# Performance work log

Measured on AMD Instinct MI355X. Metric: run time of the kernel, lower is better.

Reference implementation:

```python
import jax, jax.numpy as jnp
import numpy as np

B, T, D, H, L = 64, 512, 1024, 1024, 4


def setup_inputs() -> dict:
    key = jax.random.key(0)
    ks = jax.random.split(key, 7)
    s = 1.0 / np.sqrt(H)
    x = jax.random.normal(ks[0], (B, T, D), dtype=jnp.float32)
    dt = jax.random.uniform(ks[1], (B, T), dtype=jnp.float32)  # positive time deltas
    W_ih = jax.random.uniform(ks[2], (L, 3 * H, D), minval=-s, maxval=s, dtype=jnp.float32)
    W_hh = jax.random.uniform(ks[3], (L, 3 * H, H), minval=-s, maxval=s, dtype=jnp.float32)
    b_ih = jax.random.uniform(ks[4], (L, 3 * H), minval=-s, maxval=s, dtype=jnp.float32)
    b_hh = jax.random.uniform(ks[5], (L, 3 * H), minval=-s, maxval=s, dtype=jnp.float32)
    tau = jax.random.uniform(ks[6], (L, H), minval=0.5, maxval=2.0, dtype=jnp.float32)
    return {"x": x, "dt": dt, "W_ih": W_ih, "W_hh": W_hh, "b_ih": b_ih, "b_hh": b_hh, "tau": tau}


def reference(x, dt, W_ih, W_hh, b_ih, b_hh, tau):
    # x: [B,T,D], dt: [B,T]; stacked per-layer params: W_ih [L,3H,D], W_hh [L,3H,H],
    # b_ih/b_hh [L,3H], tau [L,H] (learned time constants, 'exp' scaling).
    n_layers = W_hh.shape[0]
    hid = W_hh.shape[2]
    inv_tau = 1.0 / jax.nn.softplus(tau)  # [L,H]

    def step(h, xt):
        # h: [B,L,H]; x_t: [B,D]; dt_t: [B]
        x_t, dt_t = xt
        inp = x_t
        new_h = []
        for i in range(n_layers):  # fixed small layer count
            decay = jnp.exp(-dt_t[:, None] * inv_tau[i])        # [B,H] exp time scaling
            hd = h[:, i] * decay
            gx = inp @ W_ih[i].T + b_ih[i]                       # [B,3H]
            gh = hd @ W_hh[i].T + b_hh[i]                        # [B,3H]
            xr, xz, xn = jnp.split(gx, 3, axis=-1)
            hr, hz, hn = jnp.split(gh, 3, axis=-1)
            r = jax.nn.sigmoid(xr + hr)
            z = jax.nn.sigmoid(xz + hz)
            n = jnp.tanh(xn + r * hn)
            h_i = (1.0 - z) * n + z * hd                         # torch GRU convention
            new_h.append(h_i)
            inp = h_i
        return jnp.stack(new_h, axis=1), new_h[-1]

    h0 = jnp.zeros((x.shape[0], n_layers, hid), dtype=x.dtype)
    xs = (jnp.swapaxes(x, 0, 1), jnp.swapaxes(dt, 0, 1))  # time-major for scan
    _, seq = jax.lax.scan(step, h0, xs)                    # seq: [T,B,H]
    return jnp.swapaxes(seq, 0, 1)                         # [B,T,H]
```

## Files before the change

kernel.cpp:

```cpp
#include <hip/hip_runtime.h>

typedef _Float16 f16;
typedef _Float16 half8 __attribute__((ext_vector_type(8)));
typedef float f32x4 __attribute__((ext_vector_type(4)));
typedef float f32x2 __attribute__((ext_vector_type(2)));

#define TT 512
#define HID 1024

#define GLOAD_LDS16(gp, lp) \
  __builtin_amdgcn_global_load_lds((const __attribute__((address_space(1))) void*)(gp), \
                                   (__attribute__((address_space(3))) void*)(lp), 16, 0, 0)

__device__ __forceinline__ half8 cvt8(f32x4 lo, f32x4 hi) {
  half8 r;
  r[0]=(f16)lo[0]; r[1]=(f16)lo[1]; r[2]=(f16)lo[2]; r[3]=(f16)lo[3];
  r[4]=(f16)hi[0]; r[5]=(f16)hi[1]; r[6]=(f16)hi[2]; r[7]=(f16)hi[3];
  return r;
}
__device__ __forceinline__ void st_sc_u32(unsigned* p, unsigned v) {
  asm volatile("global_store_dword %0, %1, off sc0 sc1" :: "v"(p), "v"(v) : "memory");
}
__device__ __forceinline__ unsigned ld_sc_u32(const unsigned* p) {
  unsigned v;
  asm volatile("global_load_dword %0, %1, off sc0 sc1\n\ts_waitcnt vmcnt(0)"
               : "=v"(v) : "v"(p) : "memory");
  return v;
}
__device__ __forceinline__ void spinFlag(const unsigned* p) {
  int gd = 0;
  while (ld_sc_u32(p) == 0u) { __builtin_amdgcn_s_sleep(1); if (++gd > (1<<20)) break; }
}
__device__ __forceinline__ float sigm(float x)  { return 1.f/(1.f + __expf(-x)); }
__device__ __forceinline__ float ftanh(float x) { return 1.f - 2.f/(1.f + __expf(2.f*x)); }

__global__ void init_misc(const float* __restrict__ x, f16* __restrict__ xh) {
  size_t i = ((size_t)blockIdx.x*256 + threadIdx.x)*8;
  f32x4 a = *(const f32x4*)(x+i);
  f32x4 b = *(const f32x4*)(x+i+4);
  *(half8*)(xh+i) = cvt8(a,b);
}

__global__ __launch_bounds__(512, 2) void tsgru_k(
    const float* __restrict__ dtp, const float* __restrict__ Wih,
    const float* __restrict__ Whh, const float* __restrict__ bih,
    const float* __restrict__ bhh, const float* __restrict__ tau,
    const f16* __restrict__ xh, f16* __restrict__ H, f16* __restrict__ HD,
    unsigned* __restrict__ flags, float* __restrict__ out) {
  extern __shared__ char lds[];
  float* PART = (float*)lds;

  const int tid = threadIdx.x, lane = tid & 63, wv = tid >> 6;
  const int g = wv >> 2, kq = wv & 3;
  const int wg = blockIdx.x, layer = wg >> 6, wgl = wg & 63, col0 = wgl*16;
  const int l5 = lane >> 5, su = lane & 31;

  const float* Wsrc = (g ? Whh : Wih) + (size_t)layer*3072*HID;
  const int wrow = col0 + (lane & 15);
  const int kfr = kq*32 + ((lane>>4)&3)*8;
  half8 bW[3][8];
  #pragma unroll
  for (int q=0;q<3;q++)
    #pragma unroll
    for (int kc=0;kc<8;kc++) {
      const float* p = Wsrc + (size_t)(q*HID + wrow)*HID + kc*128 + kfr;
      bW[q][kc] = cvt8(*(const f32x4*)p, *(const f32x4*)(p+4));
    }

  const int gb = tid >> 3, gc2 = (tid & 7)*2;
  float biR[2],biZ[2],biN[2],bhR[2],bhZ[2],bhN[2],ni[2];
  #pragma unroll
  for (int e=0;e<2;e++) {
    const int c = col0 + gc2 + e;
    biR[e]=bih[layer*3072+c]; biZ[e]=bih[layer*3072+1024+c]; biN[e]=bih[layer*3072+2048+c];
    bhR[e]=bhh[layer*3072+c]; bhZ[e]=bhh[layer*3072+1024+c]; bhN[e]=bhh[layer*3072+2048+c];
    ni[e] = -1.0f / log1pf(expf(tau[layer*HID + c]));
  }

  const f16* agB; size_t agRS;
  if (layer == 0) { agB = xh; agRS = (size_t)TT*HID; }
  else            { agB = H + (size_t)(layer-1)*TT*65536; agRS = (size_t)HID; }
  f16* HDl = HD + (size_t)layer*2*65536;
  unsigned* flagOwn = flags + (size_t)layer*TT*64;
  const unsigned* flagUp = flags + (size_t)(layer>0 ? layer-1 : 0)*TT*64;

  float hdv0 = 0.f, hdv1 = 0.f;

  for (int t = 0; t < TT; ++t) {
    const float dtg1 = (t < TT-1) ? dtp[gb*TT + t + 1] : 0.f;

    if (t > 0 && lane != wgl) spinFlag(flagOwn + (size_t)(t-1)*64 + lane);
    if (layer > 0)            spinFlag(flagUp  + (size_t)t*64 + lane);

    const f16* agT = (layer==0) ? agB + (size_t)t*HID : agB + (size_t)t*65536;
    const f16* ahT = HDl + (size_t)(t & 1)*65536;

    auto issueQ = [&](int q, int par) {
      const int qo = q*256;
      #pragma unroll
      for (int i=0;i<4;i++) {
        const int b  = wv*8 + 2*i + l5;
        const int sw = (su ^ (2*i + l5)) * 8;
        char* ld0 = lds + par*32768 + (wv*8 + 2*i)*512;
        GLOAD_LDS16(agT + (size_t)b*agRS + qo + sw, ld0);
        GLOAD_LDS16(ahT + (size_t)b*HID  + qo + sw, ld0 + 65536);
      }
    };

    issueQ(0,0); issueQ(1,1);
    asm volatile("s_waitcnt vmcnt(8)" ::: "memory");
    __builtin_amdgcn_s_barrier();

    f32x4 acc[4][3];
    #pragma unroll
    for (int m=0;m<4;m++) { acc[m][0]=(f32x4){0.f,0.f,0.f,0.f}; acc[m][1]=acc[m][0]; acc[m][2]=acc[m][0]; }

    const char* AbB = lds + (g ? 65536 : 0);
    #pragma unroll
    for (int q=0;q<4;q++) {
      const char* Ab = AbB + (q&1)*32768;
      #pragma unroll
      for (int kcq=0;kcq<2;kcq++) {
        const int ub = kcq*16 + kq*4 + ((lane>>4)&3);
        const int kc = q*2 + kcq;
        #pragma unroll
        for (int m=0;m<4;m++) {
          const int row = m*16 + (lane&15);
          const half8 aF = *(const half8*)(Ab + row*512 + ((ub ^ (row&7))*16));
          acc[m][0] = __builtin_amdgcn_mfma_f32_16x16x32_f16(aF, bW[0][kc], acc[m][0],0,0,0);
          acc[m][1] = __builtin_amdgcn_mfma_f32_16x16x32_f16(aF, bW[1][kc], acc[m][1],0,0,0);
          acc[m][2] = __builtin_amdgcn_mfma_f32_16x16x32_f16(aF, bW[2][kc], acc[m][2],0,0,0);
        }
      }
      if (q < 2) {
        __builtin_amdgcn_s_barrier();
        issueQ(q+2, q&1);
        asm volatile("s_waitcnt vmcnt(8)" ::: "memory");
        __builtin_amdgcn_s_barrier();
      } else if (q == 2) {
        asm volatile("s_waitcnt vmcnt(0)" ::: "memory");
        __builtin_amdgcn_s_barrier();
      }
    }
    __builtin_amdgcn_s_barrier();

    {
      float* Pb = PART + (size_t)((g*4+kq)*3)*1088 + (lane&15)*68 + ((lane>>4)&3)*4;
      #pragma unroll
      for (int qg=0;qg<3;qg++)
        #pragma unroll
        for (int m=0;m<4;m++)
          *(f32x4*)(Pb + qg*1088 + m*16) = acc[m][qg];
    }
    asm volatile("s_waitcnt lgkmcnt(0)" ::: "memory");
    __builtin_amdgcn_s_barrier();

    {
      float hv[2];
      #pragma unroll
      for (int e=0;e<2;e++) {
        const int pb = (gc2+e)*68 + gb;
        float sx0=0,sx1=0,sx2=0,sh0=0,sh1=0,sh2=0;
        #pragma unroll
        for (int k2=0;k2<4;k2++) {
          const float* Px = PART + (size_t)(k2*3)*1088 + pb;
          sx0 += Px[0]; sx1 += Px[1088]; sx2 += Px[2176];
          const float* Ph = PART + (size_t)((4+k2)*3)*1088 + pb;
          sh0 += Ph[0]; sh1 += Ph[1088]; sh2 += Ph[2176];
        }
        const float hdv = e ? hdv1 : hdv0;
        const float r = sigm(sx0 + biR[e] + sh0 + bhR[e]);
        const float z = sigm(sx1 + biZ[e] + sh1 + bhZ[e]);
        const float n = ftanh(sx2 + biN[e] + r*(sh2 + bhN[e]));
        hv[e] = (1.f - z)*n + z*hdv;
      }
      union { f16 h[2]; unsigned u; } pk;
      if (layer < 3) {
        pk.h[0]=(f16)hv[0]; pk.h[1]=(f16)hv[1];
        st_sc_u32((unsigned*)(H + ((size_t)layer*TT + t)*65536 + gb*HID + col0 + gc2), pk.u);
      } else {
        f32x2 v; v[0]=hv[0]; v[1]=hv[1];
        *(f32x2*)(out + ((size_t)gb*TT + t)*HID + col0 + gc2) = v;
      }
      if (t < TT-1) {
        const float hd0 = hv[0]*__expf(dtg1*ni[0]);
        const float hd1 = hv[1]*__expf(dtg1*ni[1]);
        pk.h[0]=(f16)hd0; pk.h[1]=(f16)hd1;
        st_sc_u32((unsigned*)(HDl + (size_t)((t+1)&1)*65536 + gb*HID + col0 + gc2), pk.u);
        hdv0 = hd0; hdv1 = hd1;
      }
    }
    asm volatile("s_waitcnt vmcnt(0) lgkmcnt(0)" ::: "memory");
    __builtin_amdgcn_s_barrier();
    if (tid == 0) st_sc_u32(flagOwn + (size_t)t*64 + wgl, 1u);
  }
}

extern "C" void kernel_launch(void* const* d_in, const int* in_sizes, int n_in,
                              void* d_out, int out_size, void* d_ws, size_t ws_size,
                              hipStream_t stream) {
  const float* x   = (const float*)d_in[0];
  const float* dtp = (const float*)d_in[1];
  const float* Wih = (const float*)d_in[2];
  const float* Whh = (const float*)d_in[3];
  const float* bih = (const float*)d_in[4];
  const float* bhh = (const float*)d_in[5];
  const float* tau = (const float*)d_in[6];
  float* out = (float*)d_out;
  char* ws = (char*)d_ws;

  f16* xh = (f16*)ws;
  f16* H  = (f16*)(ws + 67108864);
  f16* HD = (f16*)(ws + 268435456);
  unsigned* flags = (unsigned*)(ws + 269484032);

  (void)hipMemsetAsync(flags, 0, 524288, stream);
  (void)hipMemsetAsync(HD, 0, 1048576, stream);
  init_misc<<<16384, 256, 0, stream>>>(x, xh);
  const int ldsBytes = 131072;
  (void)hipFuncSetAttribute((const void*)tsgru_k, hipFuncAttributeMaxDynamicSharedMemorySize, ldsBytes);
  tsgru_k<<<256, 512, ldsBytes, stream>>>(dtp, Wih, Whh, bih, bhh, tau, xh, H, HD, flags, out);
}
```

Before: 4.928 ms.

## Load GRU A-operands directly to registers and decouple input/hidden wave waits

Replaces the LDS-staged global_load_lds pipeline (with its per-quarter barriers) with per-wave direct global loads of A fragments into registers, software-prefetched three k-chunks ahead. Input-projection waves now wait only on the upstream layer flag and hidden-projection waves only on their own layer's previous-step flags, so the x-side GEMM can proceed without waiting for the recurrence. The HD ring buffer grows from 2 to 8 slots so producers can run ahead without overwriting data still being read, and LDS allocation shrinks to the partial-sum buffer. The cost is uncoalesced, unswizzled global/L2 reads per wave and more register pressure.

After: 6.358 ms. 1.29x slower.

```diff
diff --git a/kernel.cpp b/kernel.cpp
--- a/kernel.cpp
+++ b/kernel.cpp
@@ -7,10 +7,6 @@
 
 #define TT 512
 #define HID 1024
-
-#define GLOAD_LDS16(gp, lp) \
-  __builtin_amdgcn_global_load_lds((const __attribute__((address_space(1))) void*)(gp), \
-                                   (__attribute__((address_space(3))) void*)(lp), 16, 0, 0)
 
 __device__ __forceinline__ half8 cvt8(f32x4 lo, f32x4 hi) {
   half8 r;
@@ -53,7 +49,6 @@
   const int tid = threadIdx.x, lane = tid & 63, wv = tid >> 6;
   const int g = wv >> 2, kq = wv & 3;
   const int wg = blockIdx.x, layer = wg >> 6, wgl = wg & 63, col0 = wgl*16;
-  const int l5 = lane >> 5, su = lane & 31;
 
   const float* Wsrc = (g ? Whh : Wih) + (size_t)layer*3072*HID;
   const int wrow = col0 + (lane & 15);
@@ -77,10 +72,9 @@
     ni[e] = -1.0f / log1pf(expf(tau[layer*HID + c]));
   }
 
-  const f16* agB; size_t agRS;
-  if (layer == 0) { agB = xh; agRS = (size_t)TT*HID; }
-  else            { agB = H + (size_t)(layer-1)*TT*65536; agRS = (size_t)HID; }
-  f16* HDl = HD + (size_t)layer*2*65536;
+  const f16* AgPlane = (layer==0) ? xh : H + (size_t)(layer-1)*TT*65536;
+  const size_t ars = g ? (size_t)HID : ((layer==0) ? (size_t)TT*HID : (size_t)HID);
+  f16* HDl = HD + (size_t)layer*8*65536;
   unsigned* flagOwn = flags + (size_t)layer*TT*64;
   const unsigned* flagUp = flags + (size_t)(layer>0 ? layer-1 : 0)*TT*64;
 
@@ -89,60 +83,48 @@
   for (int t = 0; t < TT; ++t) {
     const float dtg1 = (t < TT-1) ? dtp[gb*TT + t + 1] : 0.f;
 
-    if (t > 0 && lane != wgl) spinFlag(flagOwn + (size_t)(t-1)*64 + lane);
-    if (layer > 0)            spinFlag(flagUp  + (size_t)t*64 + lane);
-
-    const f16* agT = (layer==0) ? agB + (size_t)t*HID : agB + (size_t)t*65536;
-    const f16* ahT = HDl + (size_t)(t & 1)*65536;
-
-    auto issueQ = [&](int q, int par) {
-      const int qo = q*256;
-      #pragma unroll
-      for (int i=0;i<4;i++) {
-        const int b  = wv*8 + 2*i + l5;
-        const int sw = (su ^ (2*i + l5)) * 8;
-        char* ld0 = lds + par*32768 + (wv*8 + 2*i)*512;
-        GLOAD_LDS16(agT + (size_t)b*agRS + qo + sw, ld0);
-        GLOAD_LDS16(ahT + (size_t)b*HID  + qo + sw, ld0 + 65536);
-      }
-    };
-
-    issueQ(0,0); issueQ(1,1);
-    asm volatile("s_waitcnt vmcnt(8)" ::: "memory");
-    __builtin_amdgcn_s_barrier();
+    if (g) {
+      if (t > 0 && lane != wgl) spinFlag(flagOwn + (size_t)(t-1)*64 + lane);
+    } else if (layer > 0) {
+      spinFlag(flagUp + (size_t)t*64 + lane);
+    }
+
+    const f16* Abase = g ? (HDl + (size_t)(t&7)*65536)
+                         : ((layer==0) ? xh + (size_t)t*HID
+                                       : AgPlane + (size_t)t*65536);
+    const f16* pr[4];
+    #pragma unroll
+    for (int m=0;m<4;m++)
+      pr[m] = Abase + (size_t)(m*16 + (lane&15))*ars + kfr;
+
+    half8 aF[3][4];
+    #pragma unroll
+    for (int c=0;c<3;c++)
+      #pragma unroll
+      for (int m=0;m<4;m++)
+        aF[c][m] = *(const half8*)(pr[m] + c*128);
 
     f32x4 acc[4][3];
     #pragma unroll
-    for (int m=0;m<4;m++) { acc[m][0]=(f32x4){0.f,0.f,0.f,0.f}; acc[m][1]=acc[m][0]; acc[m][2]=acc[m][0]; }
-
-    const char* AbB = lds + (g ? 65536 : 0);
-    #pragma unroll
-    for (int q=0;q<4;q++) {
-      const char* Ab = AbB + (q&1)*32768;
-      #pragma unroll
-      for (int kcq=0;kcq<2;kcq++) {
-        const int ub = kcq*16 + kq*4 + ((lane>>4)&3);
-        const int kc = q*2 + kcq;
+    for (int m=0;m<4;m++) {
+      acc[m][0]=(f32x4){0.f,0.f,0.f,0.f}; acc[m][1]=acc[m][0]; acc[m][2]=acc[m][0];
+    }
+
+    #pragma unroll
+    for (int kc=0;kc<8;kc++) {
+      #pragma unroll
+      for (int m=0;m<4;m++) {
+        const half8 a = aF[kc%3][m];
+        acc[m][0] = __builtin_amdgcn_mfma_f32_16x16x32_f16(a, bW[0][kc], acc[m][0],0,0,0);
+        acc[m][1] = __builtin_amdgcn_mfma_f32_16x16x32_f16(a, bW[1][kc], acc[m][1],0,0,0);
+        acc[m][2] = __builtin_amdgcn_mfma_f32_16x16x32_f16(a, bW[2][kc], acc[m][2],0,0,0);
+      }
+      if (kc < 5) {
         #pragma unroll
-        for (int m=0;m<4;m++) {
-          const int row = m*16 + (lane&15);
-          const half8 aF = *(const half8*)(Ab + row*512 + ((ub ^ (row&7))*16));
-          acc[m][0] = __builtin_amdgcn_mfma_f32_16x16x32_f16(aF, bW[0][kc], acc[m][0],0,0,0);
-          acc[m][1] = __builtin_amdgcn_mfma_f32_16x16x32_f16(aF, bW[1][kc], acc[m][1],0,0,0);
-          acc[m][2] = __builtin_amdgcn_mfma_f32_16x16x32_f16(aF, bW[2][kc], acc[m][2],0,0,0);
-        }
-      }
-      if (q < 2) {
-        __builtin_amdgcn_s_barrier();
-        issueQ(q+2, q&1);
-        asm volatile("s_waitcnt vmcnt(8)" ::: "memory");
-        __builtin_amdgcn_s_barrier();
-      } else if (q == 2) {
-        asm volatile("s_waitcnt vmcnt(0)" ::: "memory");
-        __builtin_amdgcn_s_barrier();
-      }
-    }
-    __builtin_amdgcn_s_barrier();
+        for (int m=0;m<4;m++)
+          aF[(kc+3)%3][m] = *(const half8*)(pr[m] + (kc+3)*128);
+      }
+    }
 
     {
       float* Pb = PART + (size_t)((g*4+kq)*3)*1088 + (lane&15)*68 + ((lane>>4)&3)*4;
@@ -186,7 +168,7 @@
         const float hd0 = hv[0]*__expf(dtg1*ni[0]);
         const float hd1 = hv[1]*__expf(dtg1*ni[1]);
         pk.h[0]=(f16)hd0; pk.h[1]=(f16)hd1;
-        st_sc_u32((unsigned*)(HDl + (size_t)((t+1)&1)*65536 + gb*HID + col0 + gc2), pk.u);
+        st_sc_u32((unsigned*)(HDl + (size_t)((t+1)&7)*65536 + gb*HID + col0 + gc2), pk.u);
         hdv0 = hd0; hdv1 = hd1;
       }
     }
@@ -212,12 +194,12 @@
   f16* xh = (f16*)ws;
   f16* H  = (f16*)(ws + 67108864);
   f16* HD = (f16*)(ws + 268435456);
-  unsigned* flags = (unsigned*)(ws + 269484032);
+  unsigned* flags = (unsigned*)(ws + 268435456 + 4194304);
 
   (void)hipMemsetAsync(flags, 0, 524288, stream);
-  (void)hipMemsetAsync(HD, 0, 1048576, stream);
+  (void)hipMemsetAsync(HD, 0, 4194304, stream);
   init_misc<<<16384, 256, 0, stream>>>(x, xh);
-  const int ldsBytes = 131072;
+  const int ldsBytes = 104448;
   (void)hipFuncSetAttribute((const void*)tsgru_k, hipFuncAttributeMaxDynamicSharedMemorySize, ldsBytes);
   tsgru_k<<<256, 512, ldsBytes, stream>>>(dtp, Wih, Whh, bih, bhh, tau, xh, H, HD, flags, out);
 }
```
